# Kernel optimization log

Measured on AMD Instinct MI355X. Metric: run time of the kernel, lower is better.

Reference implementation:

```python
import jax, jax.numpy as jnp
import numpy as np

VOCAB, EMBED, ZCH = 4096, 128, 256
B, H, W = 32, 16, 16


def setup_inputs() -> dict:
    key = jax.random.key(0)
    k1, k2, k3, k4 = jax.random.split(key, 4)
    z_e = jax.random.normal(k1, (B, ZCH, H, W), dtype=jnp.float32)
    pre_w = jax.random.normal(k2, (EMBED, ZCH), dtype=jnp.float32) * 0.02
    pre_b = jnp.zeros((EMBED,), dtype=jnp.float32)
    # codebook initialized uniform(-1/vocab, 1/vocab) like the torch module
    emb = jax.random.uniform(k3, (VOCAB, EMBED), dtype=jnp.float32,
                             minval=-1.0 / VOCAB, maxval=1.0 / VOCAB)
    post_w = jax.random.normal(k4, (ZCH, EMBED), dtype=jnp.float32) * 0.02
    post_b = jnp.zeros((ZCH,), dtype=jnp.float32)
    return {"z_e": z_e, "pre_w": pre_w, "pre_b": pre_b, "emb": emb,
            "post_w": post_w, "post_b": post_b}


def reference(z_e, pre_w, pre_b, emb, post_w, post_b):
    # pre_quant_conv: 1x1 conv == per-pixel linear, z_channels -> embed_dim
    z = jnp.einsum('bchw,ec->behw', z_e, pre_w) + pre_b[None, :, None, None]
    b, e, h, w = z.shape
    zf = z.transpose(0, 2, 3, 1).reshape(-1, e)                 # (b*h*w, e)
    # squared distance to all codebook vectors: |z|^2 + |c|^2 - 2 z.c
    dist = (jnp.sum(zf * zf, axis=1, keepdims=True)
            + jnp.sum(emb * emb, axis=1)
            - 2.0 * zf @ emb.T)                                  # (b*h*w, vocab)
    tokens = jnp.argmin(dist, axis=-1)                           # (b*h*w,)
    z_q = emb[tokens].reshape(b, h, w, e).transpose(0, 3, 1, 2)  # (b,e,h,w)
    # straight-through estimator
    dec_in = z + jax.lax.stop_gradient(z_q - z)
    # post_quant_conv: 1x1 conv embed_dim -> z_channels (decoder input)
    rec = jnp.einsum('behw,ce->bchw', dec_in, post_w) + post_b[None, :, None, None]
    return z, z_q, rec
```

## Files before the change

### kernel.cpp

```cpp
#include <hip/hip_runtime.h>
#include <hip/hip_bf16.h>
#include <cstdint>

#define NB   32
#define NC   256
#define NE   128
#define NS   256
#define NV   4096
#define NP   8192
#define NSPLIT 4

typedef unsigned short ushort_t;
typedef __attribute__((ext_vector_type(8))) short bf16x8;
typedef __attribute__((ext_vector_type(8))) unsigned short us8;
typedef __attribute__((ext_vector_type(4))) float f32x4;

__device__ __forceinline__ float bf2f(ushort_t u) {
    union { unsigned int i; float f; } x; x.i = ((unsigned int)u) << 16; return x.f;
}
__device__ __forceinline__ ushort_t f2bf(float f) {
    __hip_bfloat16 h = __float2bfloat16(f);
    ushort_t u; __builtin_memcpy(&u, &h, 2); return u;
}

__global__ __launch_bounds__(256) void pre_conv(
    const float* __restrict__ z_e, const float* __restrict__ pre_w,
    const float* __restrict__ pre_b, float* __restrict__ out_z)
{
    __shared__ __align__(16) float wlds[16 * 256];
    const int t  = threadIdx.x;
    const int e0 = blockIdx.x * 16;
    const int b  = blockIdx.y;

    for (int idx = t; idx < 16 * 256; idx += 256) {
        int r = idx >> 8, c = idx & 255;
        wlds[r * 256 + c] = pre_w[(e0 + r) * 256 + c];
    }
    __syncthreads();

    const int s = t;
    float acc[16];
#pragma unroll
    for (int r = 0; r < 16; r++) acc[r] = pre_b[e0 + r];

    const float* zin = z_e + (size_t)(b * NC) * NS + s;
    for (int c = 0; c < NC; c += 4) {
        float z0 = zin[(c + 0) * NS];
        float z1 = zin[(c + 1) * NS];
        float z2 = zin[(c + 2) * NS];
        float z3 = zin[(c + 3) * NS];
#pragma unroll
        for (int r = 0; r < 16; r++) {
            float4 w = *(const float4*)&wlds[r * 256 + c];
            acc[r] = fmaf(z0, w.x, fmaf(z1, w.y, fmaf(z2, w.z, fmaf(z3, w.w, acc[r]))));
        }
    }
#pragma unroll
    for (int r = 0; r < 16; r++)
        out_z[(size_t)(b * NE + e0 + r) * NS + s] = acc[r];
}

__global__ __launch_bounds__(256) void pack_b(
    const float* __restrict__ emb, ushort_t* __restrict__ Bpack,
    float* __restrict__ cnorm)
{
    const int t = threadIdx.x;
    if (t >= 128) return;
    const int v = blockIdx.x * 128 + t;
    const float* row = emb + (size_t)v * NE;
    const int G = v >> 4;
    float nn = 0.f;
#pragma unroll
    for (int ks = 0; ks < 4; ks++) {
#pragma unroll
        for (int q = 0; q < 4; q++) {
            us8 hv, lv;
#pragma unroll
            for (int j = 0; j < 8; j++) {
                float x = row[ks * 32 + q * 8 + j];
                nn = fmaf(x, x, nn);
                ushort_t h = f2bf(x);
                hv[j] = h;
                lv[j] = f2bf(x - bf2f(h));
            }
            const int L = (v & 15) | (q << 4);
            *(us8*)(Bpack + ((size_t)(G * 2 + 0) * 4 + ks) * 512 + L * 8) = hv;
            *(us8*)(Bpack + ((size_t)(G * 2 + 1) * 4 + ks) * 512 + L * 8) = lv;
        }
    }
    cnorm[v] = 0.5f * nn;
}

__global__ __launch_bounds__(256, 2) void score_mfma(
    const float* __restrict__ z, const ushort_t* __restrict__ Bpack,
    const float* __restrict__ cnorm, int* __restrict__ pidx2)
{
    __shared__ __align__(16) char smraw[49152];
    float*    As  = (float*)smraw;
    float*    s1l = (float*)smraw;
    float*    s2l = (float*)(smraw + 16384);
    unsigned* iil = (unsigned*)(smraw + 32768);

    const int t = threadIdx.x;
    const int wave = t >> 6, lane = t & 63;
    const int set = blockIdx.x;
    const int split = blockIdx.y;
    const int p0 = set * 64;
    const int b  = p0 >> 8;
    const int s0 = p0 & 255;

    for (int idx = t; idx < 64 * 128; idx += 256) {
        int k = idx >> 6, i = idx & 63;
        As[i * 132 + k] = z[(size_t)(b * NE + k) * NS + s0 + i];
    }
    __syncthreads();

    bf16x8 ah[4][4], al[4][4];
    const int am = lane & 15, aq = lane >> 4;
#pragma unroll
    for (int mt = 0; mt < 4; mt++)
#pragma unroll
        for (int ks = 0; ks < 4; ks++) {
            const float* src = As + (mt * 16 + am) * 132 + ks * 32 + aq * 8;
            float4 x0 = *(const float4*)src;
            float4 x1 = *(const float4*)(src + 4);
            float xv[8] = { x0.x, x0.y, x0.z, x0.w, x1.x, x1.y, x1.z, x1.w };
            bf16x8 hv, lv;
#pragma unroll
            for (int j = 0; j < 8; j++) {
                ushort_t h = f2bf(xv[j]);
                hv[j] = (short)h;
                lv[j] = (short)f2bf(xv[j] - bf2f(h));
            }
            ah[mt][ks] = hv;
            al[mt][ks] = lv;
        }
    __syncthreads();

    float b1v[16], b2v[16]; unsigned i12[16];
#pragma unroll
    for (int i = 0; i < 16; i++) { b1v[i] = -1e30f; b2v[i] = -1e30f; i12[i] = 0u; }

    const int cg_base = split * 64 + wave * 16;

    for (int cgi = 0; cgi < 16; cgi++) {
        const int cg = cg_base + cgi;
        const ushort_t* bp = Bpack + (size_t)cg * 4096;
        bf16x8 bh[4], bl[4];
#pragma unroll
        for (int ks = 0; ks < 4; ks++) {
            bh[ks] = *(const bf16x8*)(bp + ks * 512 + lane * 8);
            bl[ks] = *(const bf16x8*)(bp + 2048 + ks * 512 + lane * 8);
        }
        const int code = cg * 16 + (lane & 15);
        const float cn = cnorm[code];

        f32x4 acc[4];
#pragma unroll
        for (int mt = 0; mt < 4; mt++) acc[mt] = (f32x4){0.f, 0.f, 0.f, 0.f};

#pragma unroll
        for (int ks = 0; ks < 4; ks++) {
#pragma unroll
            for (int mt = 0; mt < 4; mt++)
                acc[mt] = __builtin_amdgcn_mfma_f32_16x16x32_bf16(ah[mt][ks], bh[ks], acc[mt], 0, 0, 0);
#pragma unroll
            for (int mt = 0; mt < 4; mt++)
                acc[mt] = __builtin_amdgcn_mfma_f32_16x16x32_bf16(ah[mt][ks], bl[ks], acc[mt], 0, 0, 0);
#pragma unroll
            for (int mt = 0; mt < 4; mt++)
                acc[mt] = __builtin_amdgcn_mfma_f32_16x16x32_bf16(al[mt][ks], bh[ks], acc[mt], 0, 0, 0);
        }

        const unsigned chi = (unsigned)code << 16;
#pragma unroll
        for (int mt = 0; mt < 4; mt++) {
#pragma unroll
            for (int reg = 0; reg < 4; reg++) {
                const int sidx = mt * 4 + reg;
                float sc = acc[mt][reg] - cn;
                float ob1 = b1v[sidx], ob2 = b2v[sidx];
                unsigned oi = i12[sidx];
                bool gt1 = sc > ob1;
                bool gt2 = sc > ob2;
                b1v[sidx] = gt1 ? sc : ob1;
                b2v[sidx] = gt1 ? ob1 : (gt2 ? sc : ob2);
                unsigned na = chi | (oi >> 16);
                unsigned nb = (oi & 0xFFFF0000u) | (unsigned)code;
                i12[sidx] = gt1 ? na : (gt2 ? nb : oi);
            }
        }
    }

    const int res = lane & 15, quad = lane >> 4;
#pragma unroll
    for (int mt = 0; mt < 4; mt++)
#pragma unroll
        for (int reg = 0; reg < 4; reg++) {
            int px = mt * 16 + quad * 4 + reg;
            int e = (wave * 16 + res) * 64 + px;
            s1l[e] = b1v[mt * 4 + reg];
            s2l[e] = b2v[mt * 4 + reg];
            iil[e] = i12[mt * 4 + reg];
        }
    __syncthreads();

    if (t < 64) {
        float B1 = -1e30f, B2 = -1e30f;
        int   I1 = 0x7fffffff, I2 = 0x7fffffff;
        for (int w = 0; w < 64; w++) {
            int e = w * 64 + t;
            float sA = s1l[e], sB = s2l[e];
            unsigned ii = iil[e];
            int iA = (int)(ii >> 16), iB = (int)(ii & 0xffffu);
            bool a1 = (sA > B1) || (sA == B1 && iA < I1);
            bool a2 = (sA > B2) || (sA == B2 && iA < I2);
            if (a1) { B2 = B1; I2 = I1; B1 = sA; I1 = iA; }
            else if (a2) { B2 = sA; I2 = iA; }
            bool c1 = (sB > B1) || (sB == B1 && iB < I1);
            bool c2 = (sB > B2) || (sB == B2 && iB < I2);
            if (c1) { B2 = B1; I2 = I1; B1 = sB; I1 = iB; }
            else if (c2) { B2 = sB; I2 = iB; }
        }
        const int p = p0 + t;
        pidx2[(split * NP + p) * 2 + 0] = I1;
        pidx2[(split * NP + p) * 2 + 1] = I2;
    }
}

__global__ __launch_bounds__(256) void rescore_gather(
    const float* __restrict__ z, const float* __restrict__ emb,
    const int* __restrict__ pidx2, float* __restrict__ out_zq)
{
    __shared__ __align__(16) float zl[64 * 132];
    __shared__ double sc8[64 * 8];
    __shared__ int    id8[64 * 8];
    __shared__ int    tok[64];

    const int t  = threadIdx.x;
    const int p0 = blockIdx.x * 64;
    const int b  = p0 >> 8;
    const int s0 = p0 & 255;

    for (int idx = t; idx < 64 * 128; idx += 256) {
        int k = idx >> 6, i = idx & 63;
        zl[i * 132 + k] = z[(size_t)(b * NE + k) * NS + s0 + i];
    }
    __syncthreads();

    const int i_loc = t >> 2;
    const int c4    = t & 3;
    const int p     = p0 + i_loc;
#pragma unroll
    for (int cc = 0; cc < 2; cc++) {
        int ci = c4 * 2 + cc;
        int split = ci >> 1, slot = ci & 1;
        int idx = pidx2[(split * NP + p) * 2 + slot];
        const float* er = emb + (size_t)idx * NE;
        double dot = 0.0, nn = 0.0;
        for (int k = 0; k < NE; k += 4) {
            float4 e4 = *(const float4*)(er + k);
            dot += (double)zl[i_loc * 132 + k + 0] * (double)e4.x;
            dot += (double)zl[i_loc * 132 + k + 1] * (double)e4.y;
            dot += (double)zl[i_loc * 132 + k + 2] * (double)e4.z;
            dot += (double)zl[i_loc * 132 + k + 3] * (double)e4.w;
            nn  += (double)e4.x * e4.x + (double)e4.y * e4.y
                 + (double)e4.z * e4.z + (double)e4.w * e4.w;
        }
        sc8[i_loc * 8 + ci] = dot - 0.5 * nn;
        id8[i_loc * 8 + ci] = idx;
    }
    __syncthreads();

    if (t < 64) {
        double bs = -1e300; int bi = 0x7fffffff;
        for (int ci = 0; ci < 8; ci++) {
            double sc = sc8[t * 8 + ci]; int ii = id8[t * 8 + ci];
            if (sc > bs || (sc == bs && ii < bi)) { bs = sc; bi = ii; }
        }
        tok[t] = bi;
    }
    __syncthreads();

    for (int idx = t; idx < NE * 64; idx += 256) {
        int e = idx >> 6, i = idx & 63;
        out_zq[(size_t)(b * NE + e) * NS + s0 + i] = emb[(size_t)tok[i] * NE + e];
    }
}

__global__ __launch_bounds__(256) void post_conv(
    const float* __restrict__ zq, const float* __restrict__ post_w,
    const float* __restrict__ post_b, float* __restrict__ out_rec)
{
    __shared__ __align__(16) float wlds[16 * 128];
    const int t  = threadIdx.x;
    const int c0 = blockIdx.x * 16;
    const int b  = blockIdx.y;

    for (int idx = t; idx < 16 * 128; idx += 256) {
        int r = idx >> 7, e = idx & 127;
        wlds[r * 128 + e] = post_w[(c0 + r) * 128 + e];
    }
    __syncthreads();

    const int s = t;
    float acc[16];
#pragma unroll
    for (int r = 0; r < 16; r++) acc[r] = post_b[c0 + r];

    const float* zin = zq + (size_t)(b * NE) * NS + s;
    for (int e = 0; e < NE; e += 4) {
        float z0 = zin[(e + 0) * NS];
        float z1 = zin[(e + 1) * NS];
        float z2 = zin[(e + 2) * NS];
        float z3 = zin[(e + 3) * NS];
#pragma unroll
        for (int r = 0; r < 16; r++) {
            float4 w = *(const float4*)&wlds[r * 128 + e];
            acc[r] = fmaf(z0, w.x, fmaf(z1, w.y, fmaf(z2, w.z, fmaf(z3, w.w, acc[r]))));
        }
    }
#pragma unroll
    for (int r = 0; r < 16; r++)
        out_rec[(size_t)(b * NC + c0 + r) * NS + s] = acc[r];
}

extern "C" void kernel_launch(void* const* d_in, const int* in_sizes, int n_in,
                              void* d_out, int out_size, void* d_ws, size_t ws_size,
                              hipStream_t stream)
{
    const float* z_e    = (const float*)d_in[0];
    const float* pre_w  = (const float*)d_in[1];
    const float* pre_b  = (const float*)d_in[2];
    const float* emb    = (const float*)d_in[3];
    const float* post_w = (const float*)d_in[4];
    const float* post_b = (const float*)d_in[5];

    float* out     = (float*)d_out;
    float* out_z   = out;
    float* out_zq  = out + 1048576;
    float* out_rec = out + 2097152;

    const size_t NEED = (size_t)NV * NE * 2 * 2 + NV * 4 + (size_t)NSPLIT * NP * 2 * 4;
    char* scr = (ws_size >= NEED) ? (char*)d_ws : (char*)out_rec;
    ushort_t* Bpack = (ushort_t*)scr;
    float*    cnorm = (float*)(scr + 2097152);
    int*      pidx2 = (int*)(scr + 2113536);

    pre_conv      <<<dim3(8, 32),       256, 0, stream>>>(z_e, pre_w, pre_b, out_z);
    pack_b        <<<dim3(32),          256, 0, stream>>>(emb, Bpack, cnorm);
    score_mfma    <<<dim3(128, NSPLIT), 256, 0, stream>>>(out_z, Bpack, cnorm, pidx2);
    rescore_gather<<<dim3(128),         256, 0, stream>>>(out_z, emb, pidx2, out_zq);
    post_conv     <<<dim3(16, 32),      256, 0, stream>>>(out_zq, post_w, post_b, out_rec);
}
```

Baseline: 177.6 us.

## Use single-bf16 scoring with top-4 candidates and exact fp64 rescore

The candidate-scoring pass drops the split-bf16 (hi/lo) three-MFMA product and uses one bf16 MFMA with truncated A operands. It keeps a top-2 per lane using index bits packed into the float mantissa, merges them into a top-4 per pixel per split, and rescores all candidates in fp64. The split count rises to 8, occupancy to 3 blocks, and B fragments are double-buffered. Pre-conv and codebook packing are fused into one launch, and the weight LDS staging in both convs is removed. This cuts MFMA work and launch count, at the risk of missing the true argmin when bf16 error exceeds the top-4 margin.

```diff
diff --git a/kernel.cpp b/kernel.cpp
--- a/kernel.cpp
+++ b/kernel.cpp
@@ -8,7 +8,7 @@
 #define NS   256
 #define NV   4096
 #define NP   8192
-#define NSPLIT 4
+#define NSPLIT 8
 
 typedef unsigned short ushort_t;
 typedef __attribute__((ext_vector_type(8))) short bf16x8;
@@ -22,23 +22,47 @@
     __hip_bfloat16 h = __float2bfloat16(f);
     ushort_t u; __builtin_memcpy(&u, &h, 2); return u;
 }
-
-__global__ __launch_bounds__(256) void pre_conv(
+__device__ __forceinline__ unsigned asu(float f) { unsigned u; __builtin_memcpy(&u,&f,4); return u; }
+__device__ __forceinline__ float    asf(unsigned u) { float f; __builtin_memcpy(&f,&u,4); return f; }
+
+__global__ __launch_bounds__(256) void pre_conv_pack(
     const float* __restrict__ z_e, const float* __restrict__ pre_w,
-    const float* __restrict__ pre_b, float* __restrict__ out_z)
-{
-    __shared__ __align__(16) float wlds[16 * 256];
-    const int t  = threadIdx.x;
+    const float* __restrict__ pre_b, const float* __restrict__ emb,
+    float* __restrict__ out_z, ushort_t* __restrict__ Bpack,
+    float* __restrict__ cnorm)
+{
+    const int t = threadIdx.x;
+
+    if (blockIdx.x == 8) {
+        if (t < 128) {
+            const int v = blockIdx.y * 128 + t;
+            const float* row = emb + (size_t)v * NE;
+            const int G = v >> 4;
+            float nn = 0.f;
+#pragma unroll
+            for (int ks = 0; ks < 4; ks++) {
+#pragma unroll
+                for (int q = 0; q < 4; q++) {
+                    us8 hv;
+#pragma unroll
+                    for (int j = 0; j < 8; j++) {
+                        float x = row[ks * 32 + q * 8 + j];
+                        nn = fmaf(x, x, nn);
+                        hv[j] = f2bf(x);
+                    }
+                    const int L = (v & 15) | (q << 4);
+                    *(us8*)(Bpack + ((size_t)G * 4 + ks) * 512 + L * 8) = hv;
+                }
+            }
+            cnorm[v] = 0.5f * nn;
+        }
+        return;
+    }
+
     const int e0 = blockIdx.x * 16;
     const int b  = blockIdx.y;
-
-    for (int idx = t; idx < 16 * 256; idx += 256) {
-        int r = idx >> 8, c = idx & 255;
-        wlds[r * 256 + c] = pre_w[(e0 + r) * 256 + c];
-    }
-    __syncthreads();
-
-    const int s = t;
+    const int s  = t;
+
     float acc[16];
 #pragma unroll
     for (int r = 0; r < 16; r++) acc[r] = pre_b[e0 + r];
@@ -51,7 +75,7 @@
         float z3 = zin[(c + 3) * NS];
 #pragma unroll
         for (int r = 0; r < 16; r++) {
-            float4 w = *(const float4*)&wlds[r * 256 + c];
+            float4 w = *(const float4*)&pre_w[(e0 + r) * 256 + c];
             acc[r] = fmaf(z0, w.x, fmaf(z1, w.y, fmaf(z2, w.z, fmaf(z3, w.w, acc[r]))));
         }
     }
@@ -60,46 +84,15 @@
         out_z[(size_t)(b * NE + e0 + r) * NS + s] = acc[r];
 }
 
-__global__ __launch_bounds__(256) void pack_b(
-    const float* __restrict__ emb, ushort_t* __restrict__ Bpack,
-    float* __restrict__ cnorm)
-{
-    const int t = threadIdx.x;
-    if (t >= 128) return;
-    const int v = blockIdx.x * 128 + t;
-    const float* row = emb + (size_t)v * NE;
-    const int G = v >> 4;
-    float nn = 0.f;
-#pragma unroll
-    for (int ks = 0; ks < 4; ks++) {
-#pragma unroll
-        for (int q = 0; q < 4; q++) {
-            us8 hv, lv;
-#pragma unroll
-            for (int j = 0; j < 8; j++) {
-                float x = row[ks * 32 + q * 8 + j];
-                nn = fmaf(x, x, nn);
-                ushort_t h = f2bf(x);
-                hv[j] = h;
-                lv[j] = f2bf(x - bf2f(h));
-            }
-            const int L = (v & 15) | (q << 4);
-            *(us8*)(Bpack + ((size_t)(G * 2 + 0) * 4 + ks) * 512 + L * 8) = hv;
-            *(us8*)(Bpack + ((size_t)(G * 2 + 1) * 4 + ks) * 512 + L * 8) = lv;
-        }
-    }
-    cnorm[v] = 0.5f * nn;
-}
-
-__global__ __launch_bounds__(256, 2) void score_mfma(
+__global__ __launch_bounds__(256, 3) void score_mfma(
     const float* __restrict__ z, const ushort_t* __restrict__ Bpack,
-    const float* __restrict__ cnorm, int* __restrict__ pidx2)
-{
-    __shared__ __align__(16) char smraw[49152];
-    float*    As  = (float*)smraw;
-    float*    s1l = (float*)smraw;
-    float*    s2l = (float*)(smraw + 16384);
-    unsigned* iil = (unsigned*)(smraw + 32768);
+    const float* __restrict__ cnorm, int* __restrict__ pidx4)
+{
+    __shared__ __align__(16) char smraw[40960];
+    float* As  = (float*)smraw;
+    float* r1  = (float*)smraw;
+    float* r2  = (float*)(smraw + 16640);
+    float* t4b = (float*)(smraw + 33280);
 
     const int t = threadIdx.x;
     const int wave = t >> 6, lane = t & 63;
@@ -115,175 +108,178 @@
     }
     __syncthreads();
 
-    bf16x8 ah[4][4], al[4][4];
     const int am = lane & 15, aq = lane >> 4;
+    bf16x8 ah[4][4];
 #pragma unroll
     for (int mt = 0; mt < 4; mt++)
 #pragma unroll
         for (int ks = 0; ks < 4; ks++) {
-            const float* src = As + (mt * 16 + am) * 132 + ks * 32 + aq * 8;
-            float4 x0 = *(const float4*)src;
-            float4 x1 = *(const float4*)(src + 4);
-            float xv[8] = { x0.x, x0.y, x0.z, x0.w, x1.x, x1.y, x1.z, x1.w };
-            bf16x8 hv, lv;
-#pragma unroll
-            for (int j = 0; j < 8; j++) {
-                ushort_t h = f2bf(xv[j]);
-                hv[j] = (short)h;
-                lv[j] = (short)f2bf(xv[j] - bf2f(h));
-            }
-            ah[mt][ks] = hv;
-            al[mt][ks] = lv;
-        }
-    __syncthreads();
-
-    float b1v[16], b2v[16]; unsigned i12[16];
-#pragma unroll
-    for (int i = 0; i < 16; i++) { b1v[i] = -1e30f; b2v[i] = -1e30f; i12[i] = 0u; }
-
-    const int cg_base = split * 64 + wave * 16;
-
-    for (int cgi = 0; cgi < 16; cgi++) {
-        const int cg = cg_base + cgi;
-        const ushort_t* bp = Bpack + (size_t)cg * 4096;
-        bf16x8 bh[4], bl[4];
-#pragma unroll
-        for (int ks = 0; ks < 4; ks++) {
-            bh[ks] = *(const bf16x8*)(bp + ks * 512 + lane * 8);
-            bl[ks] = *(const bf16x8*)(bp + 2048 + ks * 512 + lane * 8);
-        }
-        const int code = cg * 16 + (lane & 15);
-        const float cn = cnorm[code];
+            const unsigned* src = (const unsigned*)(As + (mt * 16 + am) * 132 + ks * 32 + aq * 8);
+            union { unsigned u[4]; bf16x8 v; } pk;
+#pragma unroll
+            for (int pr = 0; pr < 4; pr++)
+                pk.u[pr] = (src[2 * pr + 1] & 0xFFFF0000u) | (src[2 * pr] >> 16);
+            ah[mt][ks] = pk.v;
+        }
+    __syncthreads();
+
+    const int Gbase = split * 32 + wave * 8;
+    float cn[8];
+#pragma unroll
+    for (int cgi = 0; cgi < 8; cgi++)
+        cn[cgi] = cnorm[(Gbase + cgi) * 16 + am];
+
+    float b1v[16], b2v[16];
+#pragma unroll
+    for (int i = 0; i < 16; i++) { b1v[i] = -1e30f; b2v[i] = -1e30f; }
+
+    bf16x8 bh[4], bhn[4];
+#pragma unroll
+    for (int ks = 0; ks < 4; ks++)
+        bh[ks] = *(const bf16x8*)(Bpack + ((size_t)Gbase * 4 + ks) * 512 + lane * 8);
+
+    for (int cgi = 0; cgi < 8; cgi++) {
+        if (cgi < 7) {
+#pragma unroll
+            for (int ks = 0; ks < 4; ks++)
+                bhn[ks] = *(const bf16x8*)(Bpack + ((size_t)(Gbase + cgi + 1) * 4 + ks) * 512 + lane * 8);
+        }
 
         f32x4 acc[4];
 #pragma unroll
         for (int mt = 0; mt < 4; mt++) acc[mt] = (f32x4){0.f, 0.f, 0.f, 0.f};
-
-#pragma unroll
-        for (int ks = 0; ks < 4; ks++) {
+#pragma unroll
+        for (int ks = 0; ks < 4; ks++)
 #pragma unroll
             for (int mt = 0; mt < 4; mt++)
                 acc[mt] = __builtin_amdgcn_mfma_f32_16x16x32_bf16(ah[mt][ks], bh[ks], acc[mt], 0, 0, 0);
-#pragma unroll
-            for (int mt = 0; mt < 4; mt++)
-                acc[mt] = __builtin_amdgcn_mfma_f32_16x16x32_bf16(ah[mt][ks], bl[ks], acc[mt], 0, 0, 0);
-#pragma unroll
-            for (int mt = 0; mt < 4; mt++)
-                acc[mt] = __builtin_amdgcn_mfma_f32_16x16x32_bf16(al[mt][ks], bh[ks], acc[mt], 0, 0, 0);
-        }
-
-        const unsigned chi = (unsigned)code << 16;
-#pragma unroll
-        for (int mt = 0; mt < 4; mt++) {
+
+#pragma unroll
+        for (int mt = 0; mt < 4; mt++)
 #pragma unroll
             for (int reg = 0; reg < 4; reg++) {
-                const int sidx = mt * 4 + reg;
-                float sc = acc[mt][reg] - cn;
-                float ob1 = b1v[sidx], ob2 = b2v[sidx];
-                unsigned oi = i12[sidx];
-                bool gt1 = sc > ob1;
-                bool gt2 = sc > ob2;
-                b1v[sidx] = gt1 ? sc : ob1;
-                b2v[sidx] = gt1 ? ob1 : (gt2 ? sc : ob2);
-                unsigned na = chi | (oi >> 16);
-                unsigned nb = (oi & 0xFFFF0000u) | (unsigned)code;
-                i12[sidx] = gt1 ? na : (gt2 ? nb : oi);
+                const int si = mt * 4 + reg;
+                float sc = acc[mt][reg] - cn[cgi];
+                float ev = asf((asu(sc) & ~7u) | (unsigned)cgi);
+                b2v[si] = fmaxf(b2v[si], fminf(ev, b1v[si]));
+                b1v[si] = fmaxf(b1v[si], ev);
             }
-        }
-    }
-
-    const int res = lane & 15, quad = lane >> 4;
+#pragma unroll
+        for (int ks = 0; ks < 4; ks++) bh[ks] = bhn[ks];
+    }
+
+    const int slot = wave * 16 + am;
 #pragma unroll
     for (int mt = 0; mt < 4; mt++)
 #pragma unroll
         for (int reg = 0; reg < 4; reg++) {
-            int px = mt * 16 + quad * 4 + reg;
-            int e = (wave * 16 + res) * 64 + px;
-            s1l[e] = b1v[mt * 4 + reg];
-            s2l[e] = b2v[mt * 4 + reg];
-            iil[e] = i12[mt * 4 + reg];
-        }
+            int px = mt * 16 + aq * 4 + reg;
+            r1[slot * 65 + px] = b1v[mt * 4 + reg];
+            r2[slot * 65 + px] = b2v[mt * 4 + reg];
+        }
+    __syncthreads();
+
+    {
+        const int px = t >> 2, ch = t & 3;
+        float t1 = -1e30f, t2 = -1e30f, t3 = -1e30f, t4 = -1e30f;
+        for (int i = 0; i < 16; i++) {
+            int sl = ch * 16 + i;
+#pragma unroll
+            for (int e = 0; e < 2; e++) {
+                float raw = e ? r2[sl * 65 + px] : r1[sl * 65 + px];
+                unsigned vb = asu(raw);
+                float v = asf((vb & ~511u) | ((unsigned)sl << 3) | (vb & 7u));
+                t4 = fmaxf(t4, fminf(v, t3));
+                t3 = fmaxf(t3, fminf(v, t2));
+                t2 = fmaxf(t2, fminf(v, t1));
+                t1 = fmaxf(t1, v);
+            }
+        }
+        float* dst = t4b + (px * 4 + ch) * 4;
+        dst[0] = t1; dst[1] = t2; dst[2] = t3; dst[3] = t4;
+    }
     __syncthreads();
 
     if (t < 64) {
-        float B1 = -1e30f, B2 = -1e30f;
-        int   I1 = 0x7fffffff, I2 = 0x7fffffff;
-        for (int w = 0; w < 64; w++) {
-            int e = w * 64 + t;
-            float sA = s1l[e], sB = s2l[e];
-            unsigned ii = iil[e];
-            int iA = (int)(ii >> 16), iB = (int)(ii & 0xffffu);
-            bool a1 = (sA > B1) || (sA == B1 && iA < I1);
-            bool a2 = (sA > B2) || (sA == B2 && iA < I2);
-            if (a1) { B2 = B1; I2 = I1; B1 = sA; I1 = iA; }
-            else if (a2) { B2 = sA; I2 = iA; }
-            bool c1 = (sB > B1) || (sB == B1 && iB < I1);
-            bool c2 = (sB > B2) || (sB == B2 && iB < I2);
-            if (c1) { B2 = B1; I2 = I1; B1 = sB; I1 = iB; }
-            else if (c2) { B2 = sB; I2 = iB; }
+        float u1 = -1e30f, u2 = -1e30f, u3 = -1e30f, u4 = -1e30f;
+        for (int ch = 0; ch < 4; ch++) {
+#pragma unroll
+            for (int j = 0; j < 4; j++) {
+                float v = t4b[(t * 4 + ch) * 4 + j];
+                u4 = fmaxf(u4, fminf(v, u3));
+                u3 = fmaxf(u3, fminf(v, u2));
+                u2 = fmaxf(u2, fminf(v, u1));
+                u1 = fmaxf(u1, v);
+            }
         }
         const int p = p0 + t;
-        pidx2[(split * NP + p) * 2 + 0] = I1;
-        pidx2[(split * NP + p) * 2 + 1] = I2;
+        float uu[4] = { u1, u2, u3, u4 };
+#pragma unroll
+        for (int j = 0; j < 4; j++) {
+            unsigned bits = asu(uu[j]) & 511u;
+            int w = (int)(bits >> 7), res = (int)((bits >> 3) & 15u), cg = (int)(bits & 7u);
+            pidx4[((size_t)split * NP + p) * 4 + j] = split * 512 + (w * 8 + cg) * 16 + res;
+        }
     }
 }
 
 __global__ __launch_bounds__(256) void rescore_gather(
     const float* __restrict__ z, const float* __restrict__ emb,
-    const int* __restrict__ pidx2, float* __restrict__ out_zq)
-{
-    __shared__ __align__(16) float zl[64 * 132];
-    __shared__ double sc8[64 * 8];
-    __shared__ int    id8[64 * 8];
-    __shared__ int    tok[64];
+    const int* __restrict__ pidx4, float* __restrict__ out_zq)
+{
+    __shared__ __align__(16) float zl[32 * 132];
+    __shared__ double bsl[32 * 8];
+    __shared__ int    bil[32 * 8];
+    __shared__ int    tok[32];
 
     const int t  = threadIdx.x;
-    const int p0 = blockIdx.x * 64;
+    const int p0 = blockIdx.x * 32;
     const int b  = p0 >> 8;
     const int s0 = p0 & 255;
 
-    for (int idx = t; idx < 64 * 128; idx += 256) {
-        int k = idx >> 6, i = idx & 63;
+    for (int idx = t; idx < 32 * 128; idx += 256) {
+        int k = idx >> 5, i = idx & 31;
         zl[i * 132 + k] = z[(size_t)(b * NE + k) * NS + s0 + i];
     }
     __syncthreads();
 
-    const int i_loc = t >> 2;
-    const int c4    = t & 3;
-    const int p     = p0 + i_loc;
-#pragma unroll
-    for (int cc = 0; cc < 2; cc++) {
-        int ci = c4 * 2 + cc;
-        int split = ci >> 1, slot = ci & 1;
-        int idx = pidx2[(split * NP + p) * 2 + slot];
+    const int il = t >> 3;
+    const int ch = t & 7;
+    const int p  = p0 + il;
+    double bs = -1e300; int bi = 0x7fffffff;
+#pragma unroll
+    for (int j = 0; j < 4; j++) {
+        int idx = pidx4[((size_t)ch * NP + p) * 4 + j];
         const float* er = emb + (size_t)idx * NE;
         double dot = 0.0, nn = 0.0;
         for (int k = 0; k < NE; k += 4) {
             float4 e4 = *(const float4*)(er + k);
-            dot += (double)zl[i_loc * 132 + k + 0] * (double)e4.x;
-            dot += (double)zl[i_loc * 132 + k + 1] * (double)e4.y;
-            dot += (double)zl[i_loc * 132 + k + 2] * (double)e4.z;
-            dot += (double)zl[i_loc * 132 + k + 3] * (double)e4.w;
+            dot += (double)zl[il * 132 + k + 0] * (double)e4.x;
+            dot += (double)zl[il * 132 + k + 1] * (double)e4.y;
+            dot += (double)zl[il * 132 + k + 2] * (double)e4.z;
+            dot += (double)zl[il * 132 + k + 3] * (double)e4.w;
             nn  += (double)e4.x * e4.x + (double)e4.y * e4.y
                  + (double)e4.z * e4.z + (double)e4.w * e4.w;
         }
-        sc8[i_loc * 8 + ci] = dot - 0.5 * nn;
-        id8[i_loc * 8 + ci] = idx;
-    }
-    __syncthreads();
-
-    if (t < 64) {
-        double bs = -1e300; int bi = 0x7fffffff;
-        for (int ci = 0; ci < 8; ci++) {
-            double sc = sc8[t * 8 + ci]; int ii = id8[t * 8 + ci];
-            if (sc > bs || (sc == bs && ii < bi)) { bs = sc; bi = ii; }
-        }
-        tok[t] = bi;
-    }
-    __syncthreads();
-
-    for (int idx = t; idx < NE * 64; idx += 256) {
-        int e = idx >> 6, i = idx & 63;
+        double sc = dot - 0.5 * nn;
+        if (sc > bs || (sc == bs && idx < bi)) { bs = sc; bi = idx; }
+    }
+    bsl[il * 8 + ch] = bs;
+    bil[il * 8 + ch] = bi;
+    __syncthreads();
+
+    if (t < 32) {
+        double B = -1e300; int I = 0x7fffffff;
+        for (int c = 0; c < 8; c++) {
+            double sc = bsl[t * 8 + c]; int ii = bil[t * 8 + c];
+            if (sc > B || (sc == B && ii < I)) { B = sc; I = ii; }
+        }
+        tok[t] = I;
+    }
+    __syncthreads();
+
+    for (int idx = t; idx < NE * 32; idx += 256) {
+        int e = idx >> 5, i = idx & 31;
         out_zq[(size_t)(b * NE + e) * NS + s0 + i] = emb[(size_t)tok[i] * NE + e];
     }
 }
@@ -292,18 +288,11 @@
     const float* __restrict__ zq, const float* __restrict__ post_w,
     const float* __restrict__ post_b, float* __restrict__ out_rec)
 {
-    __shared__ __align__(16) float wlds[16 * 128];
     const int t  = threadIdx.x;
     const int c0 = blockIdx.x * 16;
     const int b  = blockIdx.y;
-
-    for (int idx = t; idx < 16 * 128; idx += 256) {
-        int r = idx >> 7, e = idx & 127;
-        wlds[r * 128 + e] = post_w[(c0 + r) * 128 + e];
-    }
-    __syncthreads();
-
-    const int s = t;
+    const int s  = t;
+
     float acc[16];
 #pragma unroll
     for (int r = 0; r < 16; r++) acc[r] = post_b[c0 + r];
@@ -316,7 +305,7 @@
         float z3 = zin[(e + 3) * NS];
 #pragma unroll
         for (int r = 0; r < 16; r++) {
-            float4 w = *(const float4*)&wlds[r * 128 + e];
+            float4 w = *(const float4*)&post_w[(c0 + r) * 128 + e];
             acc[r] = fmaf(z0, w.x, fmaf(z1, w.y, fmaf(z2, w.z, fmaf(z3, w.w, acc[r]))));
         }
     }
@@ -341,15 +330,18 @@
     float* out_zq  = out + 1048576;
     float* out_rec = out + 2097152;
 
-    const size_t NEED = (size_t)NV * NE * 2 * 2 + NV * 4 + (size_t)NSPLIT * NP * 2 * 4;
+    const size_t SZ_BPACK = (size_t)256 * 4 * 512 * 2;
+    const size_t SZ_CNORM = (size_t)NV * 4;
+    const size_t SZ_PIDX4 = (size_t)NSPLIT * NP * 4 * 4;
+    const size_t NEED = SZ_BPACK + SZ_CNORM + SZ_PIDX4;
     char* scr = (ws_size >= NEED) ? (char*)d_ws : (char*)out_rec;
     ushort_t* Bpack = (ushort_t*)scr;
-    float*    cnorm = (float*)(scr + 2097152);
-    int*      pidx2 = (int*)(scr + 2113536);
-
-    pre_conv      <<<dim3(8, 32),       256, 0, stream>>>(z_e, pre_w, pre_b, out_z);
-    pack_b        <<<dim3(32),          256, 0, stream>>>(emb, Bpack, cnorm);
-    score_mfma    <<<dim3(128, NSPLIT), 256, 0, stream>>>(out_z, Bpack, cnorm, pidx2);
-    rescore_gather<<<dim3(128),         256, 0, stream>>>(out_z, emb, pidx2, out_zq);
-    post_conv     <<<dim3(16, 32),      256, 0, stream>>>(out_zq, post_w, post_b, out_rec);
-}
+    float*    cnorm = (float*)(scr + SZ_BPACK);
+    int*      pidx4 = (int*)(scr + SZ_BPACK + SZ_CNORM);
+
+    pre_conv_pack <<<dim3(9, 32),        256, 0, stream>>>(z_e, pre_w, pre_b, emb,
+                                                           out_z, Bpack, cnorm);
+    score_mfma    <<<dim3(128, NSPLIT),  256, 0, stream>>>(out_z, Bpack, cnorm, pidx4);
+    rescore_gather<<<dim3(256),          256, 0, stream>>>(out_z, emb, pidx4, out_zq);
+    post_conv     <<<dim3(16, 32),       256, 0, stream>>>(out_zq, post_w, post_b, out_rec);
+}
```

Measured after the change: 177.5 us. About the same (-0.1%).
